# Kernel optimization log

Measured on AMD Instinct MI355X. Metric: run time of the kernel, lower is better.

The kernel has to match this reference:

```python
import jax, jax.numpy as jnp
import numpy as np

N_NODES = 2048
IN_FEAT = 512
N_HIDDEN = 512   # layer1 out_features (concat over 8 heads -> 64 per head)
N_CLASSES = 256  # output layer out_features (1 head, averaged)
N_HEADS = 8
NEG_SLOPE = 0.2


def _gat_layer(h, adj, W, a, n_heads, n_hid, is_concat):
    """GraphAttentionLayer (v1) forward, dropout=0 (eval).
    e[i,j,h] = leakyrelu(attn([g_i ; g_j])) decomposes as
    leakyrelu(a_l.g_i + a_r.g_j) since attn is linear."""
    n = h.shape[0]
    g = (h @ W).reshape(n, n_heads, n_hid)           # [n, H, F']
    a_l, a_r = a[:n_hid], a[n_hid:]                  # attn weight split
    s_l = jnp.einsum('ihf,f->ih', g, a_l)            # [n, H]
    s_r = jnp.einsum('jhf,f->jh', g, a_r)            # [n, H]
    e = jax.nn.leaky_relu(s_l[:, None, :] + s_r[None, :, :], NEG_SLOPE)  # [n,n,H]
    e = jnp.where(adj == 0, -jnp.inf, e)             # adj [n,n,1] broadcasts over heads
    attn = jax.nn.softmax(e, axis=1)                 # softmax over neighbors j
    out = jnp.einsum('ijh,jhf->ihf', attn, g)        # [n, H, F']
    if is_concat:
        return out.reshape(n, n_heads * n_hid)
    return out.mean(axis=1)


def setup_inputs() -> dict:
    key = jax.random.key(0)
    ks = jax.random.split(key, 6)
    x = jax.random.normal(ks[0], (N_NODES, IN_FEAT), dtype=jnp.float32)
    adj = jax.random.randint(ks[1], (N_NODES, N_NODES, 1), 0, 2, dtype=jnp.int32)
    # self loops so every row of the softmax has at least one valid entry
    diag = jnp.arange(N_NODES)
    adj = adj.at[diag, diag, 0].set(1)
    W1 = jax.random.normal(ks[2], (IN_FEAT, N_HIDDEN), dtype=jnp.float32) / np.sqrt(IN_FEAT)
    a1 = jax.random.normal(ks[3], (2 * (N_HIDDEN // N_HEADS),), dtype=jnp.float32) / np.sqrt(2 * (N_HIDDEN // N_HEADS))
    W2 = jax.random.normal(ks[4], (N_HIDDEN, N_CLASSES), dtype=jnp.float32) / np.sqrt(N_HIDDEN)
    a2 = jax.random.normal(ks[5], (2 * N_CLASSES,), dtype=jnp.float32) / np.sqrt(2 * N_CLASSES)
    return {"x": x, "adj_mat": adj, "W1": W1, "a1": a1, "W2": W2, "a2": a2}


def reference(x, adj_mat, W1, a1, W2, a2):
    # GAT.forward with dropout=0 (eval mode)
    h = _gat_layer(x, adj_mat, W1, a1, N_HEADS, N_HIDDEN // N_HEADS, True)
    h = jax.nn.elu(h)
    out = _gat_layer(h, adj_mat, W2, a2, 1, N_CLASSES, False)
    return out
```

## Files before the change

kernel.cpp:

```cpp
#include <hip/hip_runtime.h>
#include <hip/hip_bf16.h>
#include <math.h>

#define NN 2048
#define LOG2E 1.4426950408889634f

typedef __attribute__((ext_vector_type(8))) short short8;
typedef __attribute__((ext_vector_type(4))) short s16x4;
typedef __attribute__((ext_vector_type(4))) float f32x4;

__device__ inline unsigned short f2bfu(float f) {
    __hip_bfloat16 h = __float2bfloat16(f);
    return *reinterpret_cast<const unsigned short*>(&h);
}
__device__ inline short f2bfs(float f) {
    __hip_bfloat16 h = __float2bfloat16(f);
    return *reinterpret_cast<const short*>(&h);
}
__device__ inline float bfu2f(unsigned short u) {
    return __uint_as_float(((unsigned int)u) << 16);
}

__device__ __forceinline__ void adj_task(
    const int* __restrict__ adj, unsigned long long* __restrict__ adjm, int task, int l)
{
    const int row = task >> 5, ch = task & 31;
    const int v = adj[(size_t)row * NN + ch * 64 + l];
    const unsigned long long bm = __ballot(v != 0);
    if (l == 0) adjm[task] = bm;
}

__device__ __forceinline__ void xpack_task(
    const float* __restrict__ x, unsigned short* __restrict__ axH,
    unsigned short* __restrict__ axL, int f, int l)
{
    const int gq = l >> 4, n16 = l & 15;
    const int mt = f >> 4, kt = f & 15;
    const int row = mt * 16 + n16;
    const int k0 = kt * 32 + 4 * gq;
    unsigned short uh[8], ul[8];
    #pragma unroll
    for (int eh = 0; eh < 2; ++eh) {
        const float4 v4 = *(const float4*)&x[(size_t)row * 512 + k0 + 16 * eh];
        const float vv[4] = {v4.x, v4.y, v4.z, v4.w};
        #pragma unroll
        for (int c = 0; c < 4; ++c) {
            const float v = vv[c];
            const unsigned short hi = f2bfu(v);
            uh[4 * eh + c] = hi;
            ul[4 * eh + c] = f2bfu(v - bfu2f(hi));
        }
    }
    *(short8*)&axH[(size_t)f * 512 + l * 8] = *(const short8*)uh;
    *(short8*)&axL[(size_t)f * 512 + l * 8] = *(const short8*)ul;
}

__device__ __forceinline__ void wpack_task(
    const float* __restrict__ W1, unsigned short* __restrict__ w1H, unsigned short* __restrict__ w1L,
    const float* __restrict__ W2, unsigned short* __restrict__ w2H, unsigned short* __restrict__ w2L,
    int f0, int l)
{
    const int gq = l >> 4, n16 = l & 15;
    int f = f0;
    const float* B; unsigned short *bH, *bL; int N;
    if (f < 512) { B = W1; bH = w1H; bL = w1L; N = 512; }
    else         { B = W2; bH = w2H; bL = w2L; N = 256; f -= 512; }
    const int nt = f >> 4, kt = f & 15;
    const int col = nt * 16 + n16;
    unsigned short uh[8], ul[8];
    #pragma unroll
    for (int e = 0; e < 8; ++e) {
        const int k = kt * 32 + 4 * gq + (e & 3) + 16 * (e >> 2);
        const float v = B[(size_t)k * N + col];
        const unsigned short hi = f2bfu(v);
        uh[e] = hi;
        ul[e] = f2bfu(v - bfu2f(hi));
    }
    *(short8*)&bH[(size_t)f * 512 + l * 8] = *(const short8*)uh;
    *(short8*)&bL[(size_t)f * 512 + l * 8] = *(const short8*)ul;
}

__device__ __forceinline__ void gemm_wave(
    const unsigned short* __restrict__ aH, const unsigned short* __restrict__ aL,
    const unsigned short* __restrict__ bH, const unsigned short* __restrict__ bL,
    const float* __restrict__ av, unsigned short* __restrict__ gpO,
    float* __restrict__ slO, float* __restrict__ srO,
    int dh, int NT, int mt, int cb, int l)
{
    const int gq = l >> 4, n16 = l & 15;
    const int nt0 = cb * 4;
    const size_t abase = (size_t)mt * 16 * 512 + l * 8;

    f32x4 acc[4];
    #pragma unroll
    for (int nt = 0; nt < 4; ++nt) acc[nt] = f32x4{0.f, 0.f, 0.f, 0.f};

#define GGL(aH_v, aL_v, bH_v, bL_v, kt_) do {                                    \
    const int kk_ = (kt_);                                                       \
    aH_v = *(const short8*)&aH[abase + (size_t)kk_ * 512];                       \
    aL_v = *(const short8*)&aL[abase + (size_t)kk_ * 512];                       \
    _Pragma("unroll")                                                            \
    for (int nt_ = 0; nt_ < 4; ++nt_) {                                          \
        const size_t bo_ = ((size_t)(nt0 + nt_) * 16 + kk_) * 512 + l * 8;       \
        bH_v[nt_] = *(const short8*)&bH[bo_];                                    \
        bL_v[nt_] = *(const short8*)&bL[bo_];                                    \
    }                                                                            \
} while (0)

#define GGC(aH_v, aL_v, bH_v, bL_v) do {                                         \
    _Pragma("unroll")                                                            \
    for (int nt_ = 0; nt_ < 4; ++nt_) {                                          \
        acc[nt_] = __builtin_amdgcn_mfma_f32_16x16x32_bf16(aH_v, bH_v[nt_], acc[nt_], 0, 0, 0); \
        acc[nt_] = __builtin_amdgcn_mfma_f32_16x16x32_bf16(aH_v, bL_v[nt_], acc[nt_], 0, 0, 0); \
        acc[nt_] = __builtin_amdgcn_mfma_f32_16x16x32_bf16(aL_v, bH_v[nt_], acc[nt_], 0, 0, 0); \
    }                                                                            \
} while (0)

    short8 aHa, aLa, bHa[4], bLa[4], aHb, aLb, bHb[4], bLb[4];
    GGL(aHa, aLa, bHa, bLa, 0);
    GGL(aHb, aLb, bHb, bLb, 1);
    for (int kt = 0; kt < 16; kt += 2) {
        GGC(aHa, aLa, bHa, bLa);
        if (kt + 2 < 16) GGL(aHa, aLa, bHa, bLa, kt + 2);
        GGC(aHb, aLb, bHb, bLb);
        if (kt + 3 < 16) GGL(aHb, aLb, bHb, bLb, kt + 3);
    }
#undef GGL
#undef GGC

    #pragma unroll
    for (int nt = 0; nt < 4; ++nt) {
        s16x4 u;
        #pragma unroll
        for (int c = 0; c < 4; ++c) u[c] = (short)f2bfu(acc[nt][c]);
        const int f = (mt >> 1) * NT + (nt0 + nt);
        *(s16x4*)&gpO[(size_t)f * 512 + l * 8 + 4 * (mt & 1)] = u;
    }
    const float* al = av;
    const float* ar = av + dh;
    float pl[4] = {0.f, 0.f, 0.f, 0.f}, pr[4] = {0.f, 0.f, 0.f, 0.f};
    #pragma unroll
    for (int nt = 0; nt < 4; ++nt) {
        const int q = (cb * 64 + 16 * nt + n16) & (dh - 1);
        const float wl = al[q], wr_ = ar[q];
        #pragma unroll
        for (int r = 0; r < 4; ++r) { pl[r] += acc[nt][r] * wl; pr[r] += acc[nt][r] * wr_; }
    }
    #pragma unroll
    for (int r = 0; r < 4; ++r) {
        #pragma unroll
        for (int off = 1; off < 16; off <<= 1) {
            pl[r] += __shfl_xor(pl[r], off);
            pr[r] += __shfl_xor(pr[r], off);
        }
    }
    if (n16 == 0) {
        const int hbase = (dh == 64 ? cb : 0) * NN;
        #pragma unroll
        for (int r = 0; r < 4; ++r) {
            const int grow = 16 * mt + 4 * gq + r;
            atomicAdd(&slO[hbase + grow], pl[r] * LOG2E);
            atomicAdd(&srO[hbase + grow], pr[r] * LOG2E);
        }
    }
}

template<int MT, int OUTMODE>
__device__ __forceinline__ void attn_task(
    const float* __restrict__ slv, const float* __restrict__ srv,
    const unsigned short* __restrict__ gp, const unsigned int* __restrict__ adjm32,
    float* __restrict__ out, unsigned short* __restrict__ aoH, unsigned short* __restrict__ aoL,
    int out_cols, int h, int do_elu, int ntg_total, int ib, int cb,
    float* accs_raw, float* zpf, int t)
{
    const int w = t >> 6, l = t & 63;
    const int gq = l >> 4, n16 = l & 15;
    const int i0 = ib * (MT * 16);
    const int ntg0 = cb * 4;
    const float* srh = srv + (size_t)h * NN;
    int arow[MT];
    float slr[MT];
    #pragma unroll
    for (int mt = 0; mt < MT; ++mt) {
        arow[mt] = i0 + 16 * mt + n16;
        slr[mt] = slv[(size_t)h * NN + arow[mt]];
    }

    f32x4 acc[MT][4];
    float zacc[MT];
    #pragma unroll
    for (int mt = 0; mt < MT; ++mt) {
        zacc[mt] = 0.f;
        #pragma unroll
        for (int nt = 0; nt < 4; ++nt) acc[mt][nt] = f32x4{0.f, 0.f, 0.f, 0.f};
    }

#define LOADH(bf_, sr_, am_, tile_, s_) do {                                     \
    const int tl_ = (tile_);                                                     \
    _Pragma("unroll")                                                            \
    for (int nt_ = 0; nt_ < 4; ++nt_)                                            \
        bf_[nt_] = *(const short8*)&gp[                                          \
            (size_t)((2 * tl_ + (s_)) * ntg_total + ntg0 + nt_) * 512 + l * 8];  \
    _Pragma("unroll")                                                            \
    for (int hb_ = 0; hb_ < 2; ++hb_)                                            \
        sr_[hb_] = *(const f32x4*)&srh[64 * tl_ + 32 * (s_) + 16 * hb_ + 4 * gq];\
    _Pragma("unroll")                                                            \
    for (int mt_ = 0; mt_ < MT; ++mt_)                                           \
        am_[mt_] = adjm32[((size_t)arow[mt_] * 32 + tl_) * 2 + (s_)];            \
} while (0)

#define COMPH(bf_, sr_, am_) do {                                                \
    short8 af_[MT];                                                              \
    _Pragma("unroll")                                                            \
    for (int mt_ = 0; mt_ < MT; ++mt_) {                                         \
        const unsigned am32_ = am_[mt_] >> (4 * gq);                             \
        _Pragma("unroll")                                                        \
        for (int hb_ = 0; hb_ < 2; ++hb_) {                                      \
            const f32x4 s4_ = sr_[hb_];                                          \
            _Pragma("unroll")                                                    \
            for (int c_ = 0; c_ < 4; ++c_) {                                     \
                float f_ = slr[mt_] + s4_[c_];                                   \
                f_ = fmaxf(f_, 0.2f * f_);                                       \
                float wv_ = __builtin_amdgcn_exp2f(f_);                          \
                const int msk_ = (int)(am32_ << (31 - (c_ + 16 * hb_))) >> 31;   \
                wv_ = __int_as_float(__float_as_int(wv_) & msk_);                \
                zacc[mt_] += wv_;                                                \
                af_[mt_][4 * hb_ + c_] = f2bfs(wv_);                             \
            }                                                                    \
        }                                                                        \
    }                                                                            \
    _Pragma("unroll")                                                            \
    for (int mt_ = 0; mt_ < MT; ++mt_)                                           \
        _Pragma("unroll")                                                        \
        for (int nt_ = 0; nt_ < 4; ++nt_)                                        \
            acc[mt_][nt_] = __builtin_amdgcn_mfma_f32_16x16x32_bf16(             \
                af_[mt_], bf_[nt_], acc[mt_][nt_], 0, 0, 0);                     \
} while (0)

    unsigned amA[MT], amB[MT];
    f32x4 srA[2], srB[2];
    short8 bfA[4], bfB[4];

    LOADH(bfA, srA, amA, w, 0);
    LOADH(bfB, srB, amB, w, 1);
    #pragma unroll
    for (int k = 0; k < 4; ++k) {
        const int tn = (k < 3) ? (w + 8 * (k + 1)) : (w + 8 * k);
        COMPH(bfA, srA, amA);
        LOADH(bfA, srA, amA, tn, 0);
        COMPH(bfB, srB, amB);
        LOADH(bfB, srB, amB, tn, 1);
    }
#undef LOADH
#undef COMPH

    #pragma unroll
    for (int mt = 0; mt < MT; ++mt) {
        zacc[mt] += __shfl_xor(zacc[mt], 16);
        zacc[mt] += __shfl_xor(zacc[mt], 32);
    }
    if (l < 16) {
        #pragma unroll
        for (int mt = 0; mt < MT; ++mt) zpf[w * (MT * 16) + 16 * mt + l] = zacc[mt];
    }

    if constexpr (OUTMODE == 0) {
        #pragma unroll
        for (int nt = 0; nt < 4; ++nt)
            #pragma unroll
            for (int r = 0; r < 4; ++r)
                accs_raw[((w * 4 + nt) * 4 + r) * 65 + l] = acc[0][nt][r];
        __syncthreads();
        #pragma unroll
        for (int idx = 0; idx < 2; ++idx) {
            const int flat = w + 8 * idx;
            const int nt = flat >> 2, r = flat & 3;
            const int ro = 4 * gq + r;
            float z = 0.f, v = 0.f;
            #pragma unroll
            for (int jj = 0; jj < 8; ++jj) {
                z += zpf[jj * 16 + ro];
                v += accs_raw[((jj * 4 + nt) * 4 + r) * 65 + l];
            }
            float o = v / z;
            if (do_elu) o = (o > 0.f) ? o : (__builtin_amdgcn_exp2f(o * LOG2E) - 1.f);
            out[(size_t)(i0 + ro) * out_cols + cb * 64 + nt * 16 + n16] = o;
        }
    } else {
        const int mtl = w & 1, eh = (w >> 1) & 1;
        const int rowl = l & 15, colq = l >> 4;
        #pragma unroll
        for (int h2 = 0; h2 < 2; ++h2) {
            #pragma unroll
            for (int mt = 0; mt < MT; ++mt)
                #pragma unroll
                for (int ntl = 0; ntl < 2; ++ntl)
                    #pragma unroll
                    for (int r = 0; r < 4; ++r)
                        accs_raw[(((w * 2 + mt) * 2 + ntl) * 4 + r) * 65 + l] =
                            acc[mt][2 * h2 + ntl][r];
            __syncthreads();
            if (w < 4) {
                const int grow = 16 * mtl + rowl;
                float z = 0.f;
                #pragma unroll
                for (int jj = 0; jj < 8; ++jj) z += zpf[jj * 32 + grow];
                const float rz = 1.0f / z;
                unsigned short uh[4], ul[4];
                #pragma unroll
                for (int c = 0; c < 4; ++c) {
                    const int c16 = 4 * colq + c;
                    float v = 0.f;
                    #pragma unroll
                    for (int jj = 0; jj < 8; ++jj)
                        v += accs_raw[(((jj * 2 + mtl) * 2 + eh) * 4 + (rowl & 3)) * 65
                                      + (rowl >> 2) * 16 + c16];
                    float o = v * rz;
                    o = (o > 0.f) ? o : (__builtin_amdgcn_exp2f(o * LOG2E) - 1.f);
                    const unsigned short hi = f2bfu(o);
                    uh[c] = hi;
                    ul[c] = f2bfu(o - bfu2f(hi));
                }
                const int mtg = ib * 2 + mtl;
                const int kt = 2 * cb + h2;
                const size_t off = ((size_t)mtg * 16 + kt) * 512 + l * 8 + 4 * eh;
                *(s16x4*)&aoH[off] = *(const s16x4*)uh;
                *(s16x4*)&aoL[off] = *(const s16x4*)ul;
            }
            __syncthreads();
        }
    }
}

__global__ __launch_bounds__(256) void prep_k(
    float* __restrict__ zeros,
    const float* __restrict__ W1, unsigned short* __restrict__ w1H, unsigned short* __restrict__ w1L,
    const float* __restrict__ W2, unsigned short* __restrict__ w2H, unsigned short* __restrict__ w2L,
    const float* __restrict__ x, unsigned short* __restrict__ axH, unsigned short* __restrict__ axL)
{
    const int b = blockIdx.x, t = threadIdx.x, w = t >> 6, l = t & 63;
    if (b < 144) {
        zeros[b * 256 + t] = 0.f;
    } else if (b < 336) {
        wpack_task(W1, w1H, w1L, W2, w2H, w2L, (b - 144) * 4 + w, l);
    } else {
        xpack_task(x, axH, axL, (b - 336) * 4 + w, l);
    }
}

__global__ __launch_bounds__(256, 2) void gemm_k(
    const unsigned short* __restrict__ aH, const unsigned short* __restrict__ aL,
    const unsigned short* __restrict__ bH, const unsigned short* __restrict__ bL,
    const float* __restrict__ av, unsigned short* __restrict__ gpO,
    float* __restrict__ slO, float* __restrict__ srO, int dh, int NT,
    int cbmask, int cbshift, int ngemm,
    const int* __restrict__ adj, unsigned long long* __restrict__ adjm)
{
    const int t = threadIdx.x, w = t >> 6, l = t & 63;
    const int bid = blockIdx.x;
    if (bid < ngemm) {
        const int cb = bid & cbmask;
        const int mt = (bid >> cbshift) * 4 + w;
        gemm_wave(aH, aL, bH, bL, av, gpO, slO, srO, dh, NT, mt, cb, l);
    } else {
        const int ab = bid - ngemm;
        const int gwave = ab * 4 + w;
        #pragma unroll 4
        for (int i = 0; i < 16; ++i)
            adj_task(adj, adjm, gwave + 4096 * i, l);
    }
}

template<int MT, int OUTMODE>
__global__ __launch_bounds__(512, 4) void attn_k(
    const float* __restrict__ slv, const float* __restrict__ srv,
    const unsigned short* __restrict__ gp, const unsigned int* __restrict__ adjm32,
    float* __restrict__ out, unsigned short* __restrict__ aoH, unsigned short* __restrict__ aoL,
    int out_cols, int hsel, int do_elu, int ntg_total, int cbmask, int cbshift)
{
    __shared__ float accs_raw[8320];
    __shared__ float zpf[256];
    const int bid = blockIdx.x;
    const int cb = bid & cbmask;
    const int ib = bid >> cbshift;
    const int h = (hsel < 0) ? cb : hsel;
    attn_task<MT, OUTMODE>(slv, srv, gp, adjm32, out, aoH, aoL, out_cols, h, do_elu,
                           ntg_total, ib, cb, accs_raw, zpf, threadIdx.x);
}

extern "C" void kernel_launch(void* const* d_in, const int* in_sizes, int n_in,
                              void* d_out, int out_size, void* d_ws, size_t ws_size,
                              hipStream_t stream)
{
    const float* x   = (const float*)d_in[0];
    const int*   adj = (const int*)  d_in[1];
    const float* W1  = (const float*)d_in[2];
    const float* a1  = (const float*)d_in[3];
    const float* W2  = (const float*)d_in[4];
    const float* a2  = (const float*)d_in[5];
    float* outp = (float*)d_out;

    float* sl1 = (float*)d_ws;
    float* sr1 = sl1 + 8 * 2048;
    float* sl2 = sr1 + 8 * 2048;
    float* sr2 = sl2 + 2048;
    unsigned long long* adjm = (unsigned long long*)(sr2 + 2048);
    unsigned short* gp1 = (unsigned short*)(adjm + 65536);
    unsigned short* gp2 = gp1 + 2048 * 512;
    unsigned short* axH = gp2 + 1024 * 512;
    unsigned short* axL = axH + 2048 * 512;
    unsigned short* ahH = axL + 2048 * 512;
    unsigned short* ahL = ahH + 2048 * 512;
    unsigned short* w1H = ahL + 2048 * 512;
    unsigned short* w1L = w1H + 512 * 512;
    unsigned short* w2H = w1L + 512 * 512;
    unsigned short* w2L = w2H + 256 * 512;

    prep_k<<<dim3(848), 256, 0, stream>>>(sl1, W1, w1H, w1L, W2, w2H, w2L, x, axH, axL);

    gemm_k<<<dim3(1280), 256, 0, stream>>>(axH, axL, w1H, w1L, a1, gp1, sl1, sr1,
                                           64, 32, 7, 3, 256, adj, adjm);
    attn_k<2, 1><<<dim3(512), 512, 0, stream>>>(sl1, sr1, gp1, (const unsigned int*)adjm,
                                                nullptr, ahH, ahL, 512, -1, 1, 32, 7, 3);
    gemm_k<<<dim3(128), 256, 0, stream>>>(ahH, ahL, w2H, w2L, a2, gp2, sl2, sr2,
                                          256, 16, 3, 2, 128, nullptr, nullptr);
    attn_k<1, 0><<<dim3(512), 512, 0, stream>>>(sl2, sr2, gp2, (const unsigned int*)adjm,
                                                outp, nullptr, nullptr, 256, 0, 0, 16, 3, 2);
}
```

Before: 59.27 us.

## Fuse bf16 split packing into GEMM and drop prep kernel and atomics

Removes the separate prep kernel that converted x, W1 and W2 into hi/lo bf16 fragments. The GEMM now loads fp32 A and B directly and splits them into bf16 hi/lo inside the MMA loop. The per-head attention score reductions are now written as partials with plain stores instead of atomics on zeroed buffers, and layer 2 sums its 4 partials when the attention kernel loads them. This saves one launch and a workspace round trip. In exchange there is repeated conversion work, and the B operand is read as strided scalar loads, which may reduce load efficiency.

```diff
diff --git a/kernel.cpp b/kernel.cpp
--- a/kernel.cpp
+++ b/kernel.cpp
@@ -30,59 +30,11 @@
     if (l == 0) adjm[task] = bm;
 }
 
-__device__ __forceinline__ void xpack_task(
-    const float* __restrict__ x, unsigned short* __restrict__ axH,
-    unsigned short* __restrict__ axL, int f, int l)
-{
-    const int gq = l >> 4, n16 = l & 15;
-    const int mt = f >> 4, kt = f & 15;
-    const int row = mt * 16 + n16;
-    const int k0 = kt * 32 + 4 * gq;
-    unsigned short uh[8], ul[8];
-    #pragma unroll
-    for (int eh = 0; eh < 2; ++eh) {
-        const float4 v4 = *(const float4*)&x[(size_t)row * 512 + k0 + 16 * eh];
-        const float vv[4] = {v4.x, v4.y, v4.z, v4.w};
-        #pragma unroll
-        for (int c = 0; c < 4; ++c) {
-            const float v = vv[c];
-            const unsigned short hi = f2bfu(v);
-            uh[4 * eh + c] = hi;
-            ul[4 * eh + c] = f2bfu(v - bfu2f(hi));
-        }
-    }
-    *(short8*)&axH[(size_t)f * 512 + l * 8] = *(const short8*)uh;
-    *(short8*)&axL[(size_t)f * 512 + l * 8] = *(const short8*)ul;
-}
-
-__device__ __forceinline__ void wpack_task(
-    const float* __restrict__ W1, unsigned short* __restrict__ w1H, unsigned short* __restrict__ w1L,
-    const float* __restrict__ W2, unsigned short* __restrict__ w2H, unsigned short* __restrict__ w2L,
-    int f0, int l)
-{
-    const int gq = l >> 4, n16 = l & 15;
-    int f = f0;
-    const float* B; unsigned short *bH, *bL; int N;
-    if (f < 512) { B = W1; bH = w1H; bL = w1L; N = 512; }
-    else         { B = W2; bH = w2H; bL = w2L; N = 256; f -= 512; }
-    const int nt = f >> 4, kt = f & 15;
-    const int col = nt * 16 + n16;
-    unsigned short uh[8], ul[8];
-    #pragma unroll
-    for (int e = 0; e < 8; ++e) {
-        const int k = kt * 32 + 4 * gq + (e & 3) + 16 * (e >> 2);
-        const float v = B[(size_t)k * N + col];
-        const unsigned short hi = f2bfu(v);
-        uh[e] = hi;
-        ul[e] = f2bfu(v - bfu2f(hi));
-    }
-    *(short8*)&bH[(size_t)f * 512 + l * 8] = *(const short8*)uh;
-    *(short8*)&bL[(size_t)f * 512 + l * 8] = *(const short8*)ul;
-}
-
+template<int APACK>
 __device__ __forceinline__ void gemm_wave(
-    const unsigned short* __restrict__ aH, const unsigned short* __restrict__ aL,
-    const unsigned short* __restrict__ bH, const unsigned short* __restrict__ bL,
+    const unsigned short* __restrict__ aHp, const unsigned short* __restrict__ aLp,
+    const float* __restrict__ Afp,
+    const float* __restrict__ Bfp, int BN,
     const float* __restrict__ av, unsigned short* __restrict__ gpO,
     float* __restrict__ slO, float* __restrict__ srO,
     int dh, int NT, int mt, int cb, int l)
@@ -90,43 +42,74 @@
     const int gq = l >> 4, n16 = l & 15;
     const int nt0 = cb * 4;
     const size_t abase = (size_t)mt * 16 * 512 + l * 8;
+    const int arow = mt * 16 + n16;
+    const int bcol = nt0 * 16 + n16;
 
     f32x4 acc[4];
     #pragma unroll
     for (int nt = 0; nt < 4; ++nt) acc[nt] = f32x4{0.f, 0.f, 0.f, 0.f};
 
-#define GGL(aH_v, aL_v, bH_v, bL_v, kt_) do {                                    \
+#define GLOAD(aH_, aL_, a0_, a1_, bf_, kt_) do {                                 \
     const int kk_ = (kt_);                                                       \
-    aH_v = *(const short8*)&aH[abase + (size_t)kk_ * 512];                       \
-    aL_v = *(const short8*)&aL[abase + (size_t)kk_ * 512];                       \
+    if constexpr (APACK == 1) {                                                  \
+        aH_ = *(const short8*)&aHp[abase + (size_t)kk_ * 512];                   \
+        aL_ = *(const short8*)&aLp[abase + (size_t)kk_ * 512];                   \
+    } else {                                                                     \
+        a0_ = *(const f32x4*)&Afp[(size_t)arow * 512 + kk_ * 32 + 4 * gq];       \
+        a1_ = *(const f32x4*)&Afp[(size_t)arow * 512 + kk_ * 32 + 4 * gq + 16];  \
+    }                                                                            \
+    _Pragma("unroll")                                                            \
+    for (int nt_ = 0; nt_ < 4; ++nt_)                                            \
+        _Pragma("unroll")                                                        \
+        for (int e_ = 0; e_ < 8; ++e_)                                           \
+            bf_[nt_][e_] = Bfp[(size_t)(kk_ * 32 + 4 * gq + (e_ & 3)             \
+                               + 16 * (e_ >> 2)) * BN + bcol + nt_ * 16];        \
+} while (0)
+
+#define GCOMP(aH_, aL_, a0_, a1_, bf_) do {                                      \
+    short8 aHr_, aLr_;                                                           \
+    if constexpr (APACK == 1) { aHr_ = aH_; aLr_ = aL_; }                        \
+    else {                                                                       \
+        _Pragma("unroll")                                                        \
+        for (int c_ = 0; c_ < 4; ++c_) {                                         \
+            const unsigned short h0_ = f2bfu(a0_[c_]);                           \
+            const unsigned short h1_ = f2bfu(a1_[c_]);                           \
+            aHr_[c_] = (short)h0_;                                               \
+            aHr_[c_ + 4] = (short)h1_;                                           \
+            aLr_[c_] = f2bfs(a0_[c_] - bfu2f(h0_));                              \
+            aLr_[c_ + 4] = f2bfs(a1_[c_] - bfu2f(h1_));                          \
+        }                                                                        \
+    }                                                                            \
     _Pragma("unroll")                                                            \
     for (int nt_ = 0; nt_ < 4; ++nt_) {                                          \
-        const size_t bo_ = ((size_t)(nt0 + nt_) * 16 + kk_) * 512 + l * 8;       \
-        bH_v[nt_] = *(const short8*)&bH[bo_];                                    \
-        bL_v[nt_] = *(const short8*)&bL[bo_];                                    \
+        short8 bH_, bL_;                                                         \
+        _Pragma("unroll")                                                        \
+        for (int e_ = 0; e_ < 8; ++e_) {                                         \
+            const float v_ = bf_[nt_][e_];                                       \
+            const unsigned short h_ = f2bfu(v_);                                 \
+            bH_[e_] = (short)h_;                                                 \
+            bL_[e_] = f2bfs(v_ - bfu2f(h_));                                     \
+        }                                                                        \
+        acc[nt_] = __builtin_amdgcn_mfma_f32_16x16x32_bf16(aHr_, bH_, acc[nt_], 0, 0, 0); \
+        acc[nt_] = __builtin_amdgcn_mfma_f32_16x16x32_bf16(aHr_, bL_, acc[nt_], 0, 0, 0); \
+        acc[nt_] = __builtin_amdgcn_mfma_f32_16x16x32_bf16(aLr_, bH_, acc[nt_], 0, 0, 0); \
     }                                                                            \
 } while (0)
 
-#define GGC(aH_v, aL_v, bH_v, bL_v) do {                                         \
-    _Pragma("unroll")                                                            \
-    for (int nt_ = 0; nt_ < 4; ++nt_) {                                          \
-        acc[nt_] = __builtin_amdgcn_mfma_f32_16x16x32_bf16(aH_v, bH_v[nt_], acc[nt_], 0, 0, 0); \
-        acc[nt_] = __builtin_amdgcn_mfma_f32_16x16x32_bf16(aH_v, bL_v[nt_], acc[nt_], 0, 0, 0); \
-        acc[nt_] = __builtin_amdgcn_mfma_f32_16x16x32_bf16(aL_v, bH_v[nt_], acc[nt_], 0, 0, 0); \
-    }                                                                            \
-} while (0)
-
-    short8 aHa, aLa, bHa[4], bLa[4], aHb, aLb, bHb[4], bLb[4];
-    GGL(aHa, aLa, bHa, bLa, 0);
-    GGL(aHb, aLb, bHb, bLb, 1);
+    short8 aHa, aLa, aHb, aLb;
+    f32x4 a0a, a1a, a0b, a1b;
+    float bfa[4][8], bfb[4][8];
+
+    GLOAD(aHa, aLa, a0a, a1a, bfa, 0);
+    GLOAD(aHb, aLb, a0b, a1b, bfb, 1);
     for (int kt = 0; kt < 16; kt += 2) {
-        GGC(aHa, aLa, bHa, bLa);
-        if (kt + 2 < 16) GGL(aHa, aLa, bHa, bLa, kt + 2);
-        GGC(aHb, aLb, bHb, bLb);
-        if (kt + 3 < 16) GGL(aHb, aLb, bHb, bLb, kt + 3);
-    }
-#undef GGL
-#undef GGC
+        GCOMP(aHa, aLa, a0a, a1a, bfa);
+        if (kt + 2 < 16) GLOAD(aHa, aLa, a0a, a1a, bfa, kt + 2);
+        GCOMP(aHb, aLb, a0b, a1b, bfb);
+        if (kt + 3 < 16) GLOAD(aHb, aLb, a0b, a1b, bfb, kt + 3);
+    }
+#undef GLOAD
+#undef GCOMP
 
     #pragma unroll
     for (int nt = 0; nt < 4; ++nt) {
@@ -155,17 +138,40 @@
         }
     }
     if (n16 == 0) {
-        const int hbase = (dh == 64 ? cb : 0) * NN;
         #pragma unroll
         for (int r = 0; r < 4; ++r) {
             const int grow = 16 * mt + 4 * gq + r;
-            atomicAdd(&slO[hbase + grow], pl[r] * LOG2E);
-            atomicAdd(&srO[hbase + grow], pr[r] * LOG2E);
+            slO[(size_t)cb * NN + grow] = pl[r] * LOG2E;
+            srO[(size_t)cb * NN + grow] = pr[r] * LOG2E;
         }
     }
 }
 
-template<int MT, int OUTMODE>
+template<int SRP>
+__device__ __forceinline__ float load_sl(const float* __restrict__ slv, int h, int row) {
+    if constexpr (SRP == 1) {
+        return slv[(size_t)h * NN + row];
+    } else {
+        float s = 0.f;
+        #pragma unroll
+        for (int p = 0; p < SRP; ++p) s += slv[(size_t)p * NN + row];
+        return s;
+    }
+}
+template<int SRP>
+__device__ __forceinline__ f32x4 load_sr4(const float* __restrict__ srv, int h, int off) {
+    f32x4 s = *(const f32x4*)&srv[(size_t)((SRP == 1) ? h : 0) * NN + off];
+    if constexpr (SRP > 1) {
+        #pragma unroll
+        for (int p = 1; p < SRP; ++p) {
+            const f32x4 t = *(const f32x4*)&srv[(size_t)p * NN + off];
+            s += t;
+        }
+    }
+    return s;
+}
+
+template<int MT, int OUTMODE, int SRP>
 __device__ __forceinline__ void attn_task(
     const float* __restrict__ slv, const float* __restrict__ srv,
     const unsigned short* __restrict__ gp, const unsigned int* __restrict__ adjm32,
@@ -177,13 +183,12 @@
     const int gq = l >> 4, n16 = l & 15;
     const int i0 = ib * (MT * 16);
     const int ntg0 = cb * 4;
-    const float* srh = srv + (size_t)h * NN;
     int arow[MT];
     float slr[MT];
     #pragma unroll
     for (int mt = 0; mt < MT; ++mt) {
         arow[mt] = i0 + 16 * mt + n16;
-        slr[mt] = slv[(size_t)h * NN + arow[mt]];
+        slr[mt] = load_sl<SRP>(slv, h, arow[mt]);
     }
 
     f32x4 acc[MT][4];
@@ -203,7 +208,7 @@
             (size_t)((2 * tl_ + (s_)) * ntg_total + ntg0 + nt_) * 512 + l * 8];  \
     _Pragma("unroll")                                                            \
     for (int hb_ = 0; hb_ < 2; ++hb_)                                            \
-        sr_[hb_] = *(const f32x4*)&srh[64 * tl_ + 32 * (s_) + 16 * hb_ + 4 * gq];\
+        sr_[hb_] = load_sr4<SRP>(srv, h, 64 * tl_ + 32 * (s_) + 16 * hb_ + 4 * gq); \
     _Pragma("unroll")                                                            \
     for (int mt_ = 0; mt_ < MT; ++mt_)                                           \
         am_[mt_] = adjm32[((size_t)arow[mt_] * 32 + tl_) * 2 + (s_)];            \
@@ -332,60 +337,41 @@
     }
 }
 
-__global__ __launch_bounds__(256) void prep_k(
-    float* __restrict__ zeros,
-    const float* __restrict__ W1, unsigned short* __restrict__ w1H, unsigned short* __restrict__ w1L,
-    const float* __restrict__ W2, unsigned short* __restrict__ w2H, unsigned short* __restrict__ w2L,
-    const float* __restrict__ x, unsigned short* __restrict__ axH, unsigned short* __restrict__ axL)
-{
-    const int b = blockIdx.x, t = threadIdx.x, w = t >> 6, l = t & 63;
-    if (b < 144) {
-        zeros[b * 256 + t] = 0.f;
-    } else if (b < 336) {
-        wpack_task(W1, w1H, w1L, W2, w2H, w2L, (b - 144) * 4 + w, l);
+template<int APACK>
+__global__ __launch_bounds__(256, 2) void gemm_k(
+    const unsigned short* __restrict__ aHp, const unsigned short* __restrict__ aLp,
+    const float* __restrict__ Afp, const float* __restrict__ Bfp, int BN,
+    const float* __restrict__ av, unsigned short* __restrict__ gpO,
+    float* __restrict__ slO, float* __restrict__ srO,
+    int dh, int NT, int ngx,
+    const int* __restrict__ adj, unsigned long long* __restrict__ adjm)
+{
+    const int t = threadIdx.x, w = t >> 6, l = t & 63;
+    const int bx = blockIdx.x, by = blockIdx.y;
+    if (bx < ngx) {
+        gemm_wave<APACK>(aHp, aLp, Afp, Bfp, BN, av, gpO, slO, srO,
+                         dh, NT, bx * 4 + w, by, l);
     } else {
-        xpack_task(x, axH, axL, (b - 336) * 4 + w, l);
-    }
-}
-
-__global__ __launch_bounds__(256, 2) void gemm_k(
-    const unsigned short* __restrict__ aH, const unsigned short* __restrict__ aL,
-    const unsigned short* __restrict__ bH, const unsigned short* __restrict__ bL,
-    const float* __restrict__ av, unsigned short* __restrict__ gpO,
-    float* __restrict__ slO, float* __restrict__ srO, int dh, int NT,
-    int cbmask, int cbshift, int ngemm,
-    const int* __restrict__ adj, unsigned long long* __restrict__ adjm)
-{
-    const int t = threadIdx.x, w = t >> 6, l = t & 63;
-    const int bid = blockIdx.x;
-    if (bid < ngemm) {
-        const int cb = bid & cbmask;
-        const int mt = (bid >> cbshift) * 4 + w;
-        gemm_wave(aH, aL, bH, bL, av, gpO, slO, srO, dh, NT, mt, cb, l);
-    } else {
-        const int ab = bid - ngemm;
-        const int gwave = ab * 4 + w;
+        const int gwave = ((bx - ngx) * 8 + by) * 4 + w;
         #pragma unroll 4
         for (int i = 0; i < 16; ++i)
             adj_task(adj, adjm, gwave + 4096 * i, l);
     }
 }
 
-template<int MT, int OUTMODE>
+template<int MT, int OUTMODE, int SRP>
 __global__ __launch_bounds__(512, 4) void attn_k(
     const float* __restrict__ slv, const float* __restrict__ srv,
     const unsigned short* __restrict__ gp, const unsigned int* __restrict__ adjm32,
     float* __restrict__ out, unsigned short* __restrict__ aoH, unsigned short* __restrict__ aoL,
-    int out_cols, int hsel, int do_elu, int ntg_total, int cbmask, int cbshift)
+    int out_cols, int hsel, int do_elu, int ntg_total)
 {
     __shared__ float accs_raw[8320];
     __shared__ float zpf[256];
-    const int bid = blockIdx.x;
-    const int cb = bid & cbmask;
-    const int ib = bid >> cbshift;
+    const int ib = blockIdx.x, cb = blockIdx.y;
     const int h = (hsel < 0) ? cb : hsel;
-    attn_task<MT, OUTMODE>(slv, srv, gp, adjm32, out, aoH, aoL, out_cols, h, do_elu,
-                           ntg_total, ib, cb, accs_raw, zpf, threadIdx.x);
+    attn_task<MT, OUTMODE, SRP>(slv, srv, gp, adjm32, out, aoH, aoL, out_cols, h, do_elu,
+                                ntg_total, ib, cb, accs_raw, zpf, threadIdx.x);
 }
 
 extern "C" void kernel_launch(void* const* d_in, const int* in_sizes, int n_in,
@@ -400,30 +386,25 @@
     const float* a2  = (const float*)d_in[5];
     float* outp = (float*)d_out;
 
-    float* sl1 = (float*)d_ws;
-    float* sr1 = sl1 + 8 * 2048;
-    float* sl2 = sr1 + 8 * 2048;
-    float* sr2 = sl2 + 2048;
-    unsigned long long* adjm = (unsigned long long*)(sr2 + 2048);
+    float* sl1  = (float*)d_ws;
+    float* sr1  = sl1 + 8 * 2048;
+    float* sl2p = sr1 + 8 * 2048;
+    float* sr2p = sl2p + 4 * 2048;
+    unsigned long long* adjm = (unsigned long long*)(sr2p + 4 * 2048);
     unsigned short* gp1 = (unsigned short*)(adjm + 65536);
     unsigned short* gp2 = gp1 + 2048 * 512;
-    unsigned short* axH = gp2 + 1024 * 512;
-    unsigned short* axL = axH + 2048 * 512;
-    unsigned short* ahH = axL + 2048 * 512;
+    unsigned short* ahH = gp2 + 1024 * 512;
     unsigned short* ahL = ahH + 2048 * 512;
-    unsigned short* w1H = ahL + 2048 * 512;
-    unsigned short* w1L = w1H + 512 * 512;
-    unsigned short* w2H = w1L + 512 * 512;
-    unsigned short* w2L = w2H + 256 * 512;
-
-    prep_k<<<dim3(848), 256, 0, stream>>>(sl1, W1, w1H, w1L, W2, w2H, w2L, x, axH, axL);
-
-    gemm_k<<<dim3(1280), 256, 0, stream>>>(axH, axL, w1H, w1L, a1, gp1, sl1, sr1,
-                                           64, 32, 7, 3, 256, adj, adjm);
-    attn_k<2, 1><<<dim3(512), 512, 0, stream>>>(sl1, sr1, gp1, (const unsigned int*)adjm,
-                                                nullptr, ahH, ahL, 512, -1, 1, 32, 7, 3);
-    gemm_k<<<dim3(128), 256, 0, stream>>>(ahH, ahL, w2H, w2L, a2, gp2, sl2, sr2,
-                                          256, 16, 3, 2, 128, nullptr, nullptr);
-    attn_k<1, 0><<<dim3(512), 512, 0, stream>>>(sl2, sr2, gp2, (const unsigned int*)adjm,
-                                                outp, nullptr, nullptr, 256, 0, 0, 16, 3, 2);
-}
+
+    gemm_k<0><<<dim3(160, 8), 256, 0, stream>>>(
+        nullptr, nullptr, x, W1, 512, a1, gp1, sl1, sr1, 64, 32, 32, adj, adjm);
+
+    attn_k<2, 1, 1><<<dim3(64, 8), 512, 0, stream>>>(
+        sl1, sr1, gp1, (const unsigned int*)adjm, nullptr, ahH, ahL, 512, -1, 1, 32);
+
+    gemm_k<1><<<dim3(32, 4), 256, 0, stream>>>(
+        ahH, ahL, nullptr, W2, 256, a2, gp2, sl2p, sr2p, 256, 16, 32, nullptr, nullptr);
+
+    attn_k<1, 0, 4><<<dim3(128, 4), 512, 0, stream>>>(
+        sl2p, sr2p, gp2, (const unsigned int*)adjm, outp, nullptr, nullptr, 256, 0, 0, 16);
+}
```

Result: slower. 72.12 us (+21.7%).
